# Optimization experiments

Measured on AMD Instinct MI355X. Metric: run time of the kernel, lower is better.

Reference implementation:

```python
import jax, jax.numpy as jnp
import numpy as np

WIN = 7
SHIFT = 3
NH = 1  # num_heads
EPS = 1e-5


def _rel_pos_index():
    # torchvision: relative_position_index for a 7x7 window -> [49,49] in [0,169)
    coords = np.stack(np.meshgrid(np.arange(WIN), np.arange(WIN), indexing='ij')).reshape(2, -1)
    rel = (coords[:, :, None] - coords[:, None, :]).transpose(1, 2, 0)  # [49,49,2]
    rel[..., 0] += WIN - 1
    rel[..., 1] += WIN - 1
    rel[..., 0] *= 2 * WIN - 1
    return rel.sum(-1)  # [49,49]


def _attn_mask(H, W):
    # region labels for cyclic-shift masking (torchvision shifted_window_attention)
    m = np.zeros((H, W), np.int32)
    cnt = 0
    for hs in ((0, H - WIN), (H - WIN, H - SHIFT), (H - SHIFT, H)):
        for ws in ((0, W - WIN), (W - WIN, W - SHIFT), (W - SHIFT, W)):
            m[hs[0]:hs[1], ws[0]:ws[1]] = cnt
            cnt += 1
    mw = m.reshape(H // WIN, WIN, W // WIN, WIN).transpose(0, 2, 1, 3).reshape(-1, WIN * WIN)  # [nW,49]
    diff = mw[:, None, :] != mw[:, :, None]
    return np.where(diff, np.float32(-100.0), np.float32(0.0))  # [nW,49,49]


def _layernorm(x, w, b):
    mu = jnp.mean(x, -1, keepdims=True)
    var = jnp.mean(jnp.square(x - mu), -1, keepdims=True)
    return (x - mu) * jax.lax.rsqrt(var + EPS) * w + b


def setup_inputs() -> dict:
    key = jax.random.key(0)
    ks = jax.random.split(key, 8)
    B, C, H, W = 8, 96, 224, 224
    s = 0.02
    return {
        'x': jax.random.normal(ks[0], (B, C, H, W), jnp.float32),
        'norm1_w': jnp.ones((C,), jnp.float32),
        'norm1_b': jnp.zeros((C,), jnp.float32),
        'qkv_w': jax.random.normal(ks[1], (3 * C, C), jnp.float32) * s,
        'qkv_b': jnp.zeros((3 * C,), jnp.float32),
        'rel_table': jax.random.normal(ks[2], ((2 * WIN - 1) ** 2, NH), jnp.float32) * s,
        'proj_w': jax.random.normal(ks[3], (C, C), jnp.float32) * s,
        'proj_b': jnp.zeros((C,), jnp.float32),
        'norm2_w': jnp.ones((C,), jnp.float32),
        'norm2_b': jnp.zeros((C,), jnp.float32),
        'mlp_w1': jax.random.normal(ks[4], (4 * C, C), jnp.float32) * s,
        'mlp_b1': jnp.zeros((4 * C,), jnp.float32),
        'mlp_w2': jax.random.normal(ks[5], (C, 4 * C), jnp.float32) * s,
        'mlp_b2': jnp.zeros((C,), jnp.float32),
    }


def _shifted_window_attention(x, qkv_w, qkv_b, rel_table, proj_w, proj_b):
    B, H, W, C = x.shape
    hd = C // NH
    nHW = (H // WIN) * (W // WIN)
    # cyclic shift
    x = jnp.roll(x, (-SHIFT, -SHIFT), axis=(1, 2))
    # window partition -> [B*nW, 49, C]
    xw = x.reshape(B, H // WIN, WIN, W // WIN, WIN, C).transpose(0, 1, 3, 2, 4, 5)
    xw = xw.reshape(B * nHW, WIN * WIN, C)
    qkv = xw @ qkv_w.T + qkv_b  # [Bw,49,3C]
    qkv = qkv.reshape(B * nHW, WIN * WIN, 3, NH, hd).transpose(2, 0, 3, 1, 4)
    q, k, v = qkv[0], qkv[1], qkv[2]  # [Bw,NH,49,hd]
    q = q * (hd ** -0.5)
    attn = jnp.einsum('bhqd,bhkd->bhqk', q, k)
    # relative position bias
    idx = _rel_pos_index().reshape(-1)
    bias = rel_table[idx].reshape(WIN * WIN, WIN * WIN, NH).transpose(2, 0, 1)  # [NH,49,49]
    attn = attn + bias[None]
    # shift mask
    mask = jnp.asarray(_attn_mask(H, W))  # [nW,49,49]
    attn = attn.reshape(B, nHW, NH, WIN * WIN, WIN * WIN) + mask[None, :, None]
    attn = jax.nn.softmax(attn.reshape(B * nHW, NH, WIN * WIN, WIN * WIN), axis=-1)
    out = jnp.einsum('bhqk,bhkd->bhqd', attn, v)  # [Bw,NH,49,hd]
    out = out.transpose(0, 2, 1, 3).reshape(B * nHW, WIN * WIN, C)
    out = out @ proj_w.T + proj_b
    # window reverse + unshift
    out = out.reshape(B, H // WIN, W // WIN, WIN, WIN, C).transpose(0, 1, 3, 2, 4, 5).reshape(B, H, W, C)
    return jnp.roll(out, (SHIFT, SHIFT), axis=(1, 2))


def reference(x, norm1_w, norm1_b, qkv_w, qkv_b, rel_table, proj_w, proj_b,
              norm2_w, norm2_b, mlp_w1, mlp_b1, mlp_w2, mlp_b2):
    h = x.transpose(0, 2, 3, 1)  # NCHW -> NHWC
    h = h + _shifted_window_attention(_layernorm(h, norm1_w, norm1_b),
                                      qkv_w, qkv_b, rel_table, proj_w, proj_b)
    m = _layernorm(h, norm2_w, norm2_b)
    m = jax.nn.gelu(m @ mlp_w1.T + mlp_b1, approximate=False) @ mlp_w2.T + mlp_b2
    h = h + m
    return h.transpose(0, 3, 1, 2)  # NHWC -> NCHW
```

## Files before the change

kernel.cpp:

```cpp
#include <hip/hip_runtime.h>
#include <hip/hip_bf16.h>
#include <math.h>

typedef __hip_bfloat16 bf16;
typedef __bf16 bf16x8 __attribute__((ext_vector_type(8)));
typedef float  f32x4  __attribute__((ext_vector_type(4)));

#define BB 8
#define CC 96
#define HH 224
#define WW 224
#define HWPIX (HH*WW)
#define TOK 49
#define NWIN 1024
#define NTOK (BB*HH*WW)

__device__ __forceinline__ bf16x8 cvt8(const float* __restrict__ p) {
    f32x4 a = *(const f32x4*)p;
    f32x4 c = *(const f32x4*)(p + 4);
    bf16x8 r;
    r[0] = (__bf16)a[0]; r[1] = (__bf16)a[1]; r[2] = (__bf16)a[2]; r[3] = (__bf16)a[3];
    r[4] = (__bf16)c[0]; r[5] = (__bf16)c[1]; r[6] = (__bf16)c[2]; r[7] = (__bf16)c[3];
    return r;
}

__device__ __forceinline__ void load8(const float* __restrict__ p, int base,
                                      int c0, int sC, float* __restrict__ dst) {
    if (sC == 1) {
        f32x4 x = *(const f32x4*)(p + base + c0);
        f32x4 y = *(const f32x4*)(p + base + c0 + 4);
        dst[0]=x[0]; dst[1]=x[1]; dst[2]=x[2]; dst[3]=x[3];
        dst[4]=y[0]; dst[5]=y[1]; dst[6]=y[2]; dst[7]=y[3];
    } else {
        #pragma unroll
        for (int j = 0; j < 8; ++j) dst[j] = p[base + (c0 + j) * sC];
    }
}

__global__ __launch_bounds__(256) void k_nchw2nhwc(const float* __restrict__ x,
                                                   float* __restrict__ hbuf) {
    __shared__ float tile[CC][57];
    int bid = blockIdx.x;
    int wc = bid & 3;
    int bh = bid >> 2;
    int h = bh % HH;
    int b = bh / HH;
    int w0 = wc * 56;
    for (int i = threadIdx.x; i < CC*14; i += 256) {
        int c = i / 14, w4 = (i % 14) * 4;
        f32x4 v = *(const f32x4*)&x[((b*CC + c)*HH + h)*WW + w0 + w4];
        tile[c][w4+0] = v[0]; tile[c][w4+1] = v[1];
        tile[c][w4+2] = v[2]; tile[c][w4+3] = v[3];
    }
    __syncthreads();
    for (int i = threadIdx.x; i < 56*24; i += 256) {
        int w = i / 24, c4 = (i % 24) * 4;
        f32x4 v;
        v[0] = tile[c4+0][w]; v[1] = tile[c4+1][w];
        v[2] = tile[c4+2][w]; v[3] = tile[c4+3][w];
        *(f32x4*)&hbuf[((b*HH + h)*WW + w0 + w)*CC + c4] = v;
    }
}

__global__ __launch_bounds__(256) void k_attn(const float* __restrict__ inbuf,
                                              float* __restrict__ outbuf,
                                              const float* __restrict__ n1w,
                                              const float* __restrict__ n1b,
                                              const float* __restrict__ qkv_w,
                                              const float* __restrict__ qkv_b,
                                              const float* __restrict__ rel_table,
                                              const float* __restrict__ proj_w,
                                              const float* __restrict__ proj_b,
                                              int sB, int sH, int sW, int sC) {
    __shared__ __attribute__((aligned(16))) __bf16 qs [64][104];
    __shared__ __attribute__((aligned(16))) __bf16 kss[64][104];
    __shared__ __attribute__((aligned(16))) __bf16 vsT[96][72];

    const int tid  = threadIdx.x;
    const int lane = tid & 63;
    const int wv   = tid >> 6;
    const int rowm = lane & 15;
    const int quad = lane >> 4;
    const int mi   = wv >> 1;
    const int ni   = wv & 1;

    const int gi = blockIdx.x;
    const int b  = gi >> 10;
    const int wrem = gi & 1023;
    const int wy = wrem >> 5;
    const int wx = wrem & 31;

    bf16x8 afrag[2][3];
    #pragma unroll
    for (int mt = 0; mt < 2; ++mt) {
        const int tk = (2*mi + mt)*16 + rowm;
        const bool valid = (tk < TOK);
        float v[24];
        if (valid) {
            int ty = tk / 7, tx = tk - 7*ty;
            int hr = wy*7 + ty, wr = wx*7 + tx;
            int sh = hr + 3; if (sh >= HH) sh -= HH;
            int sw = wr + 3; if (sw >= WW) sw -= WW;
            int base = b*sB + sh*sH + sw*sW;
            #pragma unroll
            for (int ks = 0; ks < 3; ++ks)
                load8(inbuf, base, ks*32 + quad*8, sC, v + ks*8);
        } else {
            #pragma unroll
            for (int j = 0; j < 24; ++j) v[j] = 0.f;
        }
        float s = 0.f, s2 = 0.f;
        #pragma unroll
        for (int j = 0; j < 24; ++j) { s += v[j]; s2 += v[j]*v[j]; }
        s  += __shfl_xor(s,  16, 64);  s2 += __shfl_xor(s2, 16, 64);
        s  += __shfl_xor(s,  32, 64);  s2 += __shfl_xor(s2, 32, 64);
        float mu  = s * (1.f/96.f);
        float var = s2 * (1.f/96.f) - mu*mu;
        float rs  = rsqrtf(var + 1e-5f);
        #pragma unroll
        for (int ks = 0; ks < 3; ++ks) {
            int c0 = ks*32 + quad*8;
            f32x4 w0 = *(const f32x4*)(n1w + c0);
            f32x4 w1 = *(const f32x4*)(n1w + c0 + 4);
            f32x4 b0 = *(const f32x4*)(n1b + c0);
            f32x4 b1 = *(const f32x4*)(n1b + c0 + 4);
            bf16x8 f;
            f[0] = (__bf16)(valid ? (v[ks*8+0]-mu)*rs*w0[0]+b0[0] : 0.f);
            f[1] = (__bf16)(valid ? (v[ks*8+1]-mu)*rs*w0[1]+b0[1] : 0.f);
            f[2] = (__bf16)(valid ? (v[ks*8+2]-mu)*rs*w0[2]+b0[2] : 0.f);
            f[3] = (__bf16)(valid ? (v[ks*8+3]-mu)*rs*w0[3]+b0[3] : 0.f);
            f[4] = (__bf16)(valid ? (v[ks*8+4]-mu)*rs*w1[0]+b1[0] : 0.f);
            f[5] = (__bf16)(valid ? (v[ks*8+5]-mu)*rs*w1[1]+b1[1] : 0.f);
            f[6] = (__bf16)(valid ? (v[ks*8+6]-mu)*rs*w1[2]+b1[2] : 0.f);
            f[7] = (__bf16)(valid ? (v[ks*8+7]-mu)*rs*w1[3]+b1[3] : 0.f);
            afrag[mt][ks] = f;
        }
    }
    {
        const float qscale = 0.10206207261596577f;
        #pragma unroll 3
        for (int nt = 0; nt < 9; ++nt) {
            int j = ni*144 + nt*16 + rowm;
            const float* wr = qkv_w + j*CC + quad*8;
            bf16x8 b0 = cvt8(wr);
            bf16x8 b1 = cvt8(wr + 32);
            bf16x8 b2 = cvt8(wr + 64);
            float bias = qkv_b[j];
            #pragma unroll
            for (int mt = 0; mt < 2; ++mt) {
                f32x4 acc = (f32x4){0.f,0.f,0.f,0.f};
                acc = __builtin_amdgcn_mfma_f32_16x16x32_bf16(afrag[mt][0], b0, acc, 0,0,0);
                acc = __builtin_amdgcn_mfma_f32_16x16x32_bf16(afrag[mt][1], b1, acc, 0,0,0);
                acc = __builtin_amdgcn_mfma_f32_16x16x32_bf16(afrag[mt][2], b2, acc, 0,0,0);
                #pragma unroll
                for (int r = 0; r < 4; ++r) {
                    int tok = (2*mi+mt)*16 + quad*4 + r;
                    float val = acc[r] + bias;
                    if (j < 96)        qs [tok][j]      = (__bf16)(val * qscale);
                    else if (j < 192)  kss[tok][j-96]   = (__bf16)val;
                    else               vsT[j-192][tok]  = (__bf16)val;
                }
            }
        }
    }
    __syncthreads();

    {
        bf16x8 a0 = *(const bf16x8*)&qs[16*wv + rowm][ 0 + quad*8];
        bf16x8 a1 = *(const bf16x8*)&qs[16*wv + rowm][32 + quad*8];
        bf16x8 a2 = *(const bf16x8*)&qs[16*wv + rowm][64 + quad*8];
        f32x4 acc[4];
        int ky[4], kx[4];
        #pragma unroll
        for (int nt = 0; nt < 4; ++nt) {
            bf16x8 b0 = *(const bf16x8*)&kss[nt*16 + rowm][ 0 + quad*8];
            bf16x8 b1 = *(const bf16x8*)&kss[nt*16 + rowm][32 + quad*8];
            bf16x8 b2 = *(const bf16x8*)&kss[nt*16 + rowm][64 + quad*8];
            f32x4 t = (f32x4){0.f,0.f,0.f,0.f};
            t = __builtin_amdgcn_mfma_f32_16x16x32_bf16(a0, b0, t, 0,0,0);
            t = __builtin_amdgcn_mfma_f32_16x16x32_bf16(a1, b1, t, 0,0,0);
            t = __builtin_amdgcn_mfma_f32_16x16x32_bf16(a2, b2, t, 0,0,0);
            acc[nt] = t;
            int kt = nt*16 + rowm;
            ky[nt] = kt / 7; kx[nt] = kt - 7*ky[nt];
        }
        const bool eY = (wy == 31), eX = (wx == 31);
        #pragma unroll
        for (int r = 0; r < 4; ++r) {
            int qt = 16*wv + quad*4 + r;
            int qy = qt / 7, qx = qt - 7*qy;
            int lq = (eY ? (qy < 4 ? 3 : 6) : 0) + (eX ? (qx < 4 ? 1 : 2) : 0);
            float sv[4];
            #pragma unroll
            for (int nt = 0; nt < 4; ++nt) {
                int kt = nt*16 + rowm;
                float v = acc[nt][r];
                if (kt < TOK && qt < TOK) {
                    v += rel_table[(qy - ky[nt] + 6)*13 + (qx - kx[nt] + 6)];
                    if (eY || eX) {
                        int lk = (eY ? (ky[nt] < 4 ? 3 : 6) : 0)
                               + (eX ? (kx[nt] < 4 ? 1 : 2) : 0);
                        if (lq != lk) v -= 100.f;
                    }
                } else v = -3.0e38f;
                sv[nt] = v;
            }
            float m = fmaxf(fmaxf(sv[0], sv[1]), fmaxf(sv[2], sv[3]));
            #pragma unroll
            for (int off = 8; off; off >>= 1)
                m = fmaxf(m, __shfl_xor(m, off, 64));
            float e0 = __expf(sv[0]-m), e1 = __expf(sv[1]-m);
            float e2 = __expf(sv[2]-m), e3 = __expf(sv[3]-m);
            float s = (e0+e1)+(e2+e3);
            #pragma unroll
            for (int off = 8; off; off >>= 1)
                s += __shfl_xor(s, off, 64);
            float inv = 1.f / s;
            qs[qt][ 0 + rowm] = (__bf16)(e0*inv);
            qs[qt][16 + rowm] = (__bf16)(e1*inv);
            qs[qt][32 + rowm] = (__bf16)(e2*inv);
            qs[qt][48 + rowm] = (__bf16)(e3*inv);
        }
    }
    __syncthreads();

    {
        bf16x8 a[2][2];
        #pragma unroll
        for (int mt = 0; mt < 2; ++mt)
            #pragma unroll
            for (int ku = 0; ku < 2; ++ku)
                a[mt][ku] = *(const bf16x8*)&qs[(2*mi+mt)*16 + rowm][ku*32 + quad*8];

        #pragma unroll
        for (int nt = 0; nt < 3; ++nt) {
            int c = ni*48 + nt*16 + rowm;
            bf16x8 b0 = *(const bf16x8*)&vsT[c][ 0 + quad*8];
            bf16x8 b1 = *(const bf16x8*)&vsT[c][32 + quad*8];
            #pragma unroll
            for (int mt = 0; mt < 2; ++mt) {
                f32x4 acc = (f32x4){0.f,0.f,0.f,0.f};
                acc = __builtin_amdgcn_mfma_f32_16x16x32_bf16(a[mt][0], b0, acc, 0,0,0);
                acc = __builtin_amdgcn_mfma_f32_16x16x32_bf16(a[mt][1], b1, acc, 0,0,0);
                #pragma unroll
                for (int r = 0; r < 4; ++r)
                    kss[(2*mi+mt)*16 + quad*4 + r][c] = (__bf16)acc[r];
            }
        }
    }
    __syncthreads();

    {
        bf16x8 a[2][3];
        #pragma unroll
        for (int mt = 0; mt < 2; ++mt)
            #pragma unroll
            for (int ks = 0; ks < 3; ++ks)
                a[mt][ks] = *(const bf16x8*)&kss[(2*mi+mt)*16 + rowm][ks*32 + quad*8];

        int obase[2][4];
        #pragma unroll
        for (int mt = 0; mt < 2; ++mt)
            #pragma unroll
            for (int r = 0; r < 4; ++r) {
                int tok = (2*mi+mt)*16 + quad*4 + r;
                if (tok < TOK) {
                    int ty = tok / 7, tx = tok - 7*ty;
                    int hr = wy*7 + ty, wr2 = wx*7 + tx;
                    int sh = hr + 3; if (sh >= HH) sh -= HH;
                    int sw = wr2 + 3; if (sw >= WW) sw -= WW;
                    obase[mt][r] = b*sB + sh*sH + sw*sW;
                } else obase[mt][r] = -1;
            }

        #pragma unroll
        for (int nt = 0; nt < 3; ++nt) {
            int c = ni*48 + nt*16 + rowm;
            const float* wr = proj_w + c*CC + quad*8;
            bf16x8 b0 = cvt8(wr);
            bf16x8 b1 = cvt8(wr + 32);
            bf16x8 b2 = cvt8(wr + 64);
            float bias = proj_b[c];
            #pragma unroll
            for (int mt = 0; mt < 2; ++mt) {
                f32x4 acc = (f32x4){0.f,0.f,0.f,0.f};
                acc = __builtin_amdgcn_mfma_f32_16x16x32_bf16(a[mt][0], b0, acc, 0,0,0);
                acc = __builtin_amdgcn_mfma_f32_16x16x32_bf16(a[mt][1], b1, acc, 0,0,0);
                acc = __builtin_amdgcn_mfma_f32_16x16x32_bf16(a[mt][2], b2, acc, 0,0,0);
                #pragma unroll
                for (int r = 0; r < 4; ++r) {
                    if (obase[mt][r] >= 0) {
                        int g = obase[mt][r] + c*sC;
                        outbuf[g] = inbuf[g] + acc[r] + bias;
                    }
                }
            }
        }
    }
}

__global__ __launch_bounds__(256) void k_mlp_mfma(const float* __restrict__ buf,
                                                  float* __restrict__ out,
                                                  const float* __restrict__ n2w,
                                                  const float* __restrict__ n2b,
                                                  const float* __restrict__ w1g,
                                                  const float* __restrict__ b1g,
                                                  const float* __restrict__ w2g,
                                                  const float* __restrict__ b2g) {
    __shared__ __attribute__((aligned(16))) char smraw[36352];
    auto sW1 = (__bf16(*)[104])(smraw);
    auto sW2 = (__bf16(*)[72])(smraw + 13312);
    auto sH  = (__bf16(*)[72])(smraw + 27136);
    auto sOut = (float(*)[97])(smraw);

    const int tid  = threadIdx.x;
    const int lane = tid & 63;
    const int wv   = tid >> 6;
    const int rowm = lane & 15;
    const int quad = lane >> 4;
    const int t0   = blockIdx.x * 64;

    bf16x8 afrag[3];
    {
        const int base = (t0 + 16*wv + rowm) * CC;
        float v[24];
        #pragma unroll
        for (int ks = 0; ks < 3; ++ks) {
            f32x4 x = *(const f32x4*)(buf + base + ks*32 + quad*8);
            f32x4 y = *(const f32x4*)(buf + base + ks*32 + quad*8 + 4);
            v[ks*8+0]=x[0]; v[ks*8+1]=x[1]; v[ks*8+2]=x[2]; v[ks*8+3]=x[3];
            v[ks*8+4]=y[0]; v[ks*8+5]=y[1]; v[ks*8+6]=y[2]; v[ks*8+7]=y[3];
        }
        float s = 0.f, s2 = 0.f;
        #pragma unroll
        for (int j = 0; j < 24; ++j) { s += v[j]; s2 += v[j]*v[j]; }
        s  += __shfl_xor(s,  16, 64);  s2 += __shfl_xor(s2, 16, 64);
        s  += __shfl_xor(s,  32, 64);  s2 += __shfl_xor(s2, 32, 64);
        float mu  = s * (1.f/96.f);
        float var = s2 * (1.f/96.f) - mu*mu;
        float rs  = rsqrtf(var + 1e-5f);
        #pragma unroll
        for (int ks = 0; ks < 3; ++ks) {
            int c0 = ks*32 + quad*8;
            f32x4 w0 = *(const f32x4*)(n2w + c0);
            f32x4 w1 = *(const f32x4*)(n2w + c0 + 4);
            f32x4 b0 = *(const f32x4*)(n2b + c0);
            f32x4 b1 = *(const f32x4*)(n2b + c0 + 4);
            bf16x8 f;
            f[0] = (__bf16)((v[ks*8+0]-mu)*rs*w0[0]+b0[0]);
            f[1] = (__bf16)((v[ks*8+1]-mu)*rs*w0[1]+b0[1]);
            f[2] = (__bf16)((v[ks*8+2]-mu)*rs*w0[2]+b0[2]);
            f[3] = (__bf16)((v[ks*8+3]-mu)*rs*w0[3]+b0[3]);
            f[4] = (__bf16)((v[ks*8+4]-mu)*rs*w1[0]+b1[0]);
            f[5] = (__bf16)((v[ks*8+5]-mu)*rs*w1[1]+b1[1]);
            f[6] = (__bf16)((v[ks*8+6]-mu)*rs*w1[2]+b1[2]);
            f[7] = (__bf16)((v[ks*8+7]-mu)*rs*w1[3]+b1[3]);
            afrag[ks] = f;
        }
    }

    f32x4 acc2[6];
    #pragma unroll
    for (int nt = 0; nt < 6; ++nt) acc2[nt] = (f32x4){0.f,0.f,0.f,0.f};

    for (int ch = 0; ch < 6; ++ch) {
        __syncthreads();
        for (int g = tid; g < 768; g += 256) {
            int row = g / 12, col8 = (g % 12) * 8;
            *(bf16x8*)&sW1[row][col8] = cvt8(w1g + ch*6144 + row*96 + col8);
        }
        for (int g = tid; g < 768; g += 256) {
            int row = g / 8, col8 = (g % 8) * 8;
            *(bf16x8*)&sW2[row][col8] = cvt8(w2g + row*384 + ch*64 + col8);
        }
        __syncthreads();

        #pragma unroll
        for (int nt = 0; nt < 4; ++nt) {
            bf16x8 w0 = *(const bf16x8*)&sW1[nt*16 + rowm][ 0 + quad*8];
            bf16x8 w1v = *(const bf16x8*)&sW1[nt*16 + rowm][32 + quad*8];
            bf16x8 w2v = *(const bf16x8*)&sW1[nt*16 + rowm][64 + quad*8];
            f32x4 acc = (f32x4){0.f,0.f,0.f,0.f};
            acc = __builtin_amdgcn_mfma_f32_16x16x32_bf16(afrag[0], w0,  acc, 0,0,0);
            acc = __builtin_amdgcn_mfma_f32_16x16x32_bf16(afrag[1], w1v, acc, 0,0,0);
            acc = __builtin_amdgcn_mfma_f32_16x16x32_bf16(afrag[2], w2v, acc, 0,0,0);
            float bias = b1g[ch*64 + nt*16 + rowm];
            #pragma unroll
            for (int r = 0; r < 4; ++r) {
                float v = acc[r] + bias;
                v = 0.5f * v * (1.f + erff(v * 0.70710678118654752f));
                sH[16*wv + quad*4 + r][nt*16 + rowm] = (__bf16)v;
            }
        }

        bf16x8 h0 = *(const bf16x8*)&sH[16*wv + rowm][ 0 + quad*8];
        bf16x8 h1 = *(const bf16x8*)&sH[16*wv + rowm][32 + quad*8];
        #pragma unroll
        for (int nt = 0; nt < 6; ++nt) {
            bf16x8 w0 = *(const bf16x8*)&sW2[nt*16 + rowm][ 0 + quad*8];
            bf16x8 w1v = *(const bf16x8*)&sW2[nt*16 + rowm][32 + quad*8];
            acc2[nt] = __builtin_amdgcn_mfma_f32_16x16x32_bf16(h0, w0,  acc2[nt], 0,0,0);
            acc2[nt] = __builtin_amdgcn_mfma_f32_16x16x32_bf16(h1, w1v, acc2[nt], 0,0,0);
        }
    }

    __syncthreads();
    #pragma unroll
    for (int nt = 0; nt < 6; ++nt) {
        int c = nt*16 + rowm;
        float bias = b2g[c];
        #pragma unroll
        for (int r = 0; r < 4; ++r) {
            int t = 16*wv + quad*4 + r;
            sOut[t][c] = buf[(t0 + t)*CC + c] + acc2[nt][r] + bias;
        }
    }
    __syncthreads();
    {
        int b  = t0 / HWPIX;
        int p0 = t0 - b*HWPIX;
        for (int i = tid; i < CC*64; i += 256) {
            int c = i >> 6, t = i & 63;
            out[(b*CC + c)*HWPIX + p0 + t] = sOut[t][c];
        }
    }
}

__global__ __launch_bounds__(256) void k_mlp_s(float* __restrict__ buf,
                                               const float* __restrict__ n2w,
                                               const float* __restrict__ n2b,
                                               const float* __restrict__ w1,
                                               const float* __restrict__ b1,
                                               const float* __restrict__ w2,
                                               const float* __restrict__ b2,
                                               int sB, int sPix, int sC) {
    __shared__ float ln2[4][CC];
    __shared__ float hid[4][384];
    __shared__ float hraw[4][CC];
    __shared__ int   tbase[4];

    const int tid  = threadIdx.x;
    const int lane = tid & 63;
    const int wv   = tid >> 6;
    const int tok0 = blockIdx.x * 4;

    {
        int tok = tok0 + wv;
        int base = (tok / HWPIX)*sB + (tok % HWPIX)*sPix;
        if (lane == 0) tbase[wv] = base;
        float v0 = buf[base + lane*sC];
        float v1 = (lane < 32) ? buf[base + (64 + lane)*sC] : 0.f;
        float s  = v0 + v1;
        float s2 = v0*v0 + v1*v1;
        #pragma unroll
        for (int off = 32; off; off >>= 1) {
            s  += __shfl_down(s,  off, 64);
            s2 += __shfl_down(s2, off, 64);
        }
        s  = __shfl(s, 0, 64);
        s2 = __shfl(s2, 0, 64);
        float mu  = s * (1.f/96.f);
        float var = s2 * (1.f/96.f) - mu*mu;
        float rs  = rsqrtf(var + 1e-5f);
        hraw[wv][lane] = v0;
        ln2[wv][lane]  = (v0 - mu)*rs*n2w[lane] + n2b[lane];
        if (lane < 32) {
            hraw[wv][64+lane] = v1;
            ln2[wv][64+lane]  = (v1 - mu)*rs*n2w[64+lane] + n2b[64+lane];
        }
    }
    __syncthreads();

    for (int o = tid; o < 4*384; o += 256) {
        int ti = o / 384, j = o % 384;
        const float* wrow = w1 + j*CC;
        float acc = b1[j];
        #pragma unroll 8
        for (int c = 0; c < CC; ++c) acc += ln2[ti][c] * wrow[c];
        hid[ti][j] = 0.5f * acc * (1.f + erff(acc * 0.70710678118654752f));
    }
    __syncthreads();

    for (int o = tid; o < 4*CC; o += 256) {
        int ti = o / CC, c = o % CC;
        const float* wrow = w2 + c*384;
        float acc = b2[c];
        #pragma unroll 8
        for (int k = 0; k < 384; ++k) acc += hid[ti][k] * wrow[k];
        buf[tbase[ti] + c*sC] = hraw[ti][c] + acc;
    }
}

extern "C" void kernel_launch(void* const* d_in, const int* in_sizes, int n_in,
                              void* d_out, int out_size, void* d_ws, size_t ws_size,
                              hipStream_t stream) {
    const float* x        = (const float*)d_in[0];
    const float* norm1_w  = (const float*)d_in[1];
    const float* norm1_b  = (const float*)d_in[2];
    const float* qkv_w    = (const float*)d_in[3];
    const float* qkv_b    = (const float*)d_in[4];
    const float* rel_tab  = (const float*)d_in[5];
    const float* proj_w   = (const float*)d_in[6];
    const float* proj_b   = (const float*)d_in[7];
    const float* norm2_w  = (const float*)d_in[8];
    const float* norm2_b  = (const float*)d_in[9];
    const float* mlp_w1   = (const float*)d_in[10];
    const float* mlp_b1   = (const float*)d_in[11];
    const float* mlp_w2   = (const float*)d_in[12];
    const float* mlp_b2   = (const float*)d_in[13];
    float* out = (float*)d_out;

    const int n = BB*CC*HH*WW;
    const size_t need = (size_t)n * sizeof(float);

    dim3 blk(256);
    if (ws_size >= need) {
        float* hbuf = (float*)d_ws;
        k_nchw2nhwc<<<dim3(BB*HH*4), blk, 0, stream>>>(x, hbuf);
        k_attn<<<dim3(BB*NWIN), blk, 0, stream>>>(hbuf, hbuf,
                norm1_w, norm1_b, qkv_w, qkv_b, rel_tab, proj_w, proj_b,
                HH*WW*CC, WW*CC, CC, 1);
        k_mlp_mfma<<<dim3(NTOK/64), blk, 0, stream>>>(hbuf, out,
                norm2_w, norm2_b, mlp_w1, mlp_b1, mlp_w2, mlp_b2);
    } else {
        k_attn<<<dim3(BB*NWIN), blk, 0, stream>>>(x, out,
                norm1_w, norm1_b, qkv_w, qkv_b, rel_tab, proj_w, proj_b,
                CC*HH*WW, WW, 1, HH*WW);
        k_mlp_s<<<dim3(NTOK/4), blk, 0, stream>>>(out,
                norm2_w, norm2_b, mlp_w1, mlp_b1, mlp_w2, mlp_b2,
                CC*HH*WW, 1, HH*WW);
    }
}
```

Baseline: 888.7 us.

## Pre-convert weights to bf16 and read MLP weights directly from global

Four small conversion kernels cast the qkv, proj and MLP weights to bf16 once per call into extra workspace, and the attention and MLP kernels then load bf16 fragments directly instead of converting fp32 on the fly. The MLP kernel no longer stages weight chunks through shared memory with two barriers per chunk. It reads fragments straight from global/L2, which shrinks LDS use and may raise occupancy. The cost is four extra launches and more global/L2 fragment traffic, and the new path only runs if the workspace has room for the extra tail.

```diff
diff --git a/kernel.cpp b/kernel.cpp
--- a/kernel.cpp
+++ b/kernel.cpp
@@ -15,6 +15,8 @@
 #define NWIN 1024
 #define NTOK (BB*HH*WW)
 
+#define WTAIL_BYTES 221184
+
 __device__ __forceinline__ bf16x8 cvt8(const float* __restrict__ p) {
     f32x4 a = *(const f32x4*)p;
     f32x4 c = *(const f32x4*)(p + 4);
@@ -22,6 +24,12 @@
     r[0] = (__bf16)a[0]; r[1] = (__bf16)a[1]; r[2] = (__bf16)a[2]; r[3] = (__bf16)a[3];
     r[4] = (__bf16)c[0]; r[5] = (__bf16)c[1]; r[6] = (__bf16)c[2]; r[7] = (__bf16)c[3];
     return r;
+}
+
+__device__ __forceinline__ bf16x8 ldw8(const float* __restrict__ wf,
+                                       const __bf16* __restrict__ wb, int off) {
+    if (wb) return *(const bf16x8*)(wb + off);
+    return cvt8(wf + off);
 }
 
 __device__ __forceinline__ void load8(const float* __restrict__ p, int base,
@@ -35,6 +43,12 @@
         #pragma unroll
         for (int j = 0; j < 8; ++j) dst[j] = p[base + (c0 + j) * sC];
     }
+}
+
+__global__ __launch_bounds__(256) void k_cvt(const float* __restrict__ src,
+                                             __bf16* __restrict__ dst, int n8) {
+    int i = blockIdx.x * 256 + threadIdx.x;
+    if (i < n8) *(bf16x8*)(dst + i*8) = cvt8(src + i*8);
 }
 
 __global__ __launch_bounds__(256) void k_nchw2nhwc(const float* __restrict__ x,
@@ -71,6 +85,8 @@
                                               const float* __restrict__ rel_table,
                                               const float* __restrict__ proj_w,
                                               const float* __restrict__ proj_b,
+                                              const __bf16* __restrict__ qkv_wb,
+                                              const __bf16* __restrict__ proj_wb,
                                               int sB, int sH, int sW, int sC) {
     __shared__ __attribute__((aligned(16))) __bf16 qs [64][104];
     __shared__ __attribute__((aligned(16))) __bf16 kss[64][104];
@@ -141,10 +157,10 @@
         #pragma unroll 3
         for (int nt = 0; nt < 9; ++nt) {
             int j = ni*144 + nt*16 + rowm;
-            const float* wr = qkv_w + j*CC + quad*8;
-            bf16x8 b0 = cvt8(wr);
-            bf16x8 b1 = cvt8(wr + 32);
-            bf16x8 b2 = cvt8(wr + 64);
+            int wo = j*CC + quad*8;
+            bf16x8 b0 = ldw8(qkv_w, qkv_wb, wo);
+            bf16x8 b1 = ldw8(qkv_w, qkv_wb, wo + 32);
+            bf16x8 b2 = ldw8(qkv_w, qkv_wb, wo + 64);
             float bias = qkv_b[j];
             #pragma unroll
             for (int mt = 0; mt < 2; ++mt) {
@@ -276,10 +292,10 @@
         #pragma unroll
         for (int nt = 0; nt < 3; ++nt) {
             int c = ni*48 + nt*16 + rowm;
-            const float* wr = proj_w + c*CC + quad*8;
-            bf16x8 b0 = cvt8(wr);
-            bf16x8 b1 = cvt8(wr + 32);
-            bf16x8 b2 = cvt8(wr + 64);
+            int wo = c*CC + quad*8;
+            bf16x8 b0 = ldw8(proj_w, proj_wb, wo);
+            bf16x8 b1 = ldw8(proj_w, proj_wb, wo + 32);
+            bf16x8 b2 = ldw8(proj_w, proj_wb, wo + 64);
             float bias = proj_b[c];
             #pragma unroll
             for (int mt = 0; mt < 2; ++mt) {
@@ -306,11 +322,11 @@
                                                   const float* __restrict__ w1g,
                                                   const float* __restrict__ b1g,
                                                   const float* __restrict__ w2g,
-                                                  const float* __restrict__ b2g) {
-    __shared__ __attribute__((aligned(16))) char smraw[36352];
-    auto sW1 = (__bf16(*)[104])(smraw);
-    auto sW2 = (__bf16(*)[72])(smraw + 13312);
-    auto sH  = (__bf16(*)[72])(smraw + 27136);
+                                                  const float* __restrict__ b2g,
+                                                  const __bf16* __restrict__ w1b,
+                                                  const __bf16* __restrict__ w2b) {
+    __shared__ __attribute__((aligned(16))) char smraw[24832];
+    auto sH   = (__bf16(*)[72])(smraw);
     auto sOut = (float(*)[97])(smraw);
 
     const int tid  = threadIdx.x;
@@ -364,27 +380,18 @@
     for (int nt = 0; nt < 6; ++nt) acc2[nt] = (f32x4){0.f,0.f,0.f,0.f};
 
     for (int ch = 0; ch < 6; ++ch) {
-        __syncthreads();
-        for (int g = tid; g < 768; g += 256) {
-            int row = g / 12, col8 = (g % 12) * 8;
-            *(bf16x8*)&sW1[row][col8] = cvt8(w1g + ch*6144 + row*96 + col8);
-        }
-        for (int g = tid; g < 768; g += 256) {
-            int row = g / 8, col8 = (g % 8) * 8;
-            *(bf16x8*)&sW2[row][col8] = cvt8(w2g + row*384 + ch*64 + col8);
-        }
-        __syncthreads();
-
         #pragma unroll
         for (int nt = 0; nt < 4; ++nt) {
-            bf16x8 w0 = *(const bf16x8*)&sW1[nt*16 + rowm][ 0 + quad*8];
-            bf16x8 w1v = *(const bf16x8*)&sW1[nt*16 + rowm][32 + quad*8];
-            bf16x8 w2v = *(const bf16x8*)&sW1[nt*16 + rowm][64 + quad*8];
+            int row = ch*64 + nt*16 + rowm;
+            int wo = row*96 + quad*8;
+            bf16x8 w0  = ldw8(w1g, w1b, wo);
+            bf16x8 w1v = ldw8(w1g, w1b, wo + 32);
+            bf16x8 w2v = ldw8(w1g, w1b, wo + 64);
             f32x4 acc = (f32x4){0.f,0.f,0.f,0.f};
             acc = __builtin_amdgcn_mfma_f32_16x16x32_bf16(afrag[0], w0,  acc, 0,0,0);
             acc = __builtin_amdgcn_mfma_f32_16x16x32_bf16(afrag[1], w1v, acc, 0,0,0);
             acc = __builtin_amdgcn_mfma_f32_16x16x32_bf16(afrag[2], w2v, acc, 0,0,0);
-            float bias = b1g[ch*64 + nt*16 + rowm];
+            float bias = b1g[row];
             #pragma unroll
             for (int r = 0; r < 4; ++r) {
                 float v = acc[r] + bias;
@@ -397,8 +404,10 @@
         bf16x8 h1 = *(const bf16x8*)&sH[16*wv + rowm][32 + quad*8];
         #pragma unroll
         for (int nt = 0; nt < 6; ++nt) {
-            bf16x8 w0 = *(const bf16x8*)&sW2[nt*16 + rowm][ 0 + quad*8];
-            bf16x8 w1v = *(const bf16x8*)&sW2[nt*16 + rowm][32 + quad*8];
+            int row = nt*16 + rowm;
+            int wo = row*384 + ch*64 + quad*8;
+            bf16x8 w0  = ldw8(w2g, w2b, wo);
+            bf16x8 w1v = ldw8(w2g, w2b, wo + 32);
             acc2[nt] = __builtin_amdgcn_mfma_f32_16x16x32_bf16(h0, w0,  acc2[nt], 0,0,0);
             acc2[nt] = __builtin_amdgcn_mfma_f32_16x16x32_bf16(h1, w1v, acc2[nt], 0,0,0);
         }
@@ -516,15 +525,30 @@
     dim3 blk(256);
     if (ws_size >= need) {
         float* hbuf = (float*)d_ws;
+        __bf16* qkv_wb = nullptr; __bf16* proj_wb = nullptr;
+        __bf16* w1b = nullptr;    __bf16* w2b = nullptr;
+        if (ws_size >= need + WTAIL_BYTES) {
+            __bf16* wt = (__bf16*)((char*)d_ws + need);
+            qkv_wb  = wt;
+            proj_wb = wt + 27648;
+            w1b     = wt + 36864;
+            w2b     = wt + 73728;
+            k_cvt<<<dim3((27648/8+255)/256), blk, 0, stream>>>(qkv_w,  qkv_wb,  27648/8);
+            k_cvt<<<dim3(( 9216/8+255)/256), blk, 0, stream>>>(proj_w, proj_wb,  9216/8);
+            k_cvt<<<dim3((36864/8+255)/256), blk, 0, stream>>>(mlp_w1, w1b,     36864/8);
+            k_cvt<<<dim3((36864/8+255)/256), blk, 0, stream>>>(mlp_w2, w2b,     36864/8);
+        }
         k_nchw2nhwc<<<dim3(BB*HH*4), blk, 0, stream>>>(x, hbuf);
         k_attn<<<dim3(BB*NWIN), blk, 0, stream>>>(hbuf, hbuf,
                 norm1_w, norm1_b, qkv_w, qkv_b, rel_tab, proj_w, proj_b,
+                qkv_wb, proj_wb,
                 HH*WW*CC, WW*CC, CC, 1);
         k_mlp_mfma<<<dim3(NTOK/64), blk, 0, stream>>>(hbuf, out,
-                norm2_w, norm2_b, mlp_w1, mlp_b1, mlp_w2, mlp_b2);
+                norm2_w, norm2_b, mlp_w1, mlp_b1, mlp_w2, mlp_b2, w1b, w2b);
     } else {
         k_attn<<<dim3(BB*NWIN), blk, 0, stream>>>(x, out,
                 norm1_w, norm1_b, qkv_w, qkv_b, rel_tab, proj_w, proj_b,
+                nullptr, nullptr,
                 CC*HH*WW, WW, 1, HH*WW);
         k_mlp_s<<<dim3(NTOK/4), blk, 0, stream>>>(out,
                 norm2_w, norm2_b, mlp_w1, mlp_b1, mlp_w2, mlp_b2,
```

After: 918.8 us. 3.4% more time.
